# Performance work log

Hardware: AMD Instinct MI355X
Metric: run time of the kernel (lower is better)

The kernel has to match this reference:

```python
import jax, jax.numpy as jnp
import numpy as np

EMBED = 50
SEQ = 100
NLABEL = 15
HID = 20
VOCAB = 50000
BATCH = 8192


def gru_scan(xs, W, U, b, return_sequences):
    """Keras GRUCell (reset_after=True, gate order z,r,h).
    xs: (B, T, D). W: (D, 3H), U: (H, 3H), b: (2, 3H) [input bias, recurrent bias].
    """
    B = xs.shape[0]
    H = U.shape[0]
    bi, br = b[0], b[1]
    h0 = jnp.zeros((B, H), dtype=xs.dtype)

    def step(h, x_t):
        mx = x_t @ W + bi                      # (B, 3H)
        mh = h @ U + br                        # (B, 3H)
        xz, xr, xh = mx[:, :H], mx[:, H:2*H], mx[:, 2*H:]
        hz, hr, hh_ = mh[:, :H], mh[:, H:2*H], mh[:, 2*H:]
        z = jax.nn.sigmoid(xz + hz)
        r = jax.nn.sigmoid(xr + hr)
        hh = jnp.tanh(xh + r * hh_)
        h_new = z * h + (1.0 - z) * hh
        return h_new, h_new

    xs_t = jnp.swapaxes(xs, 0, 1)              # (T, B, D)
    h_last, hs = jax.lax.scan(step, h0, xs_t)
    if return_sequences:
        return jnp.swapaxes(hs, 0, 1)          # (B, T, H)
    return h_last                               # (B, H)


def setup_inputs() -> dict:
    key = jax.random.key(0)
    ks = jax.random.split(key, 9)
    s = 0.05
    return {
        "x": jax.random.randint(ks[0], (BATCH, SEQ), 0, VOCAB),
        "emb_table": jax.random.normal(ks[1], (VOCAB, EMBED), jnp.float32) * s,
        "W1": jax.random.normal(ks[2], (EMBED, 3 * HID), jnp.float32) * s,
        "U1": jax.random.normal(ks[3], (HID, 3 * HID), jnp.float32) * s,
        "b1": jnp.zeros((2, 3 * HID), jnp.float32),
        "W2": jax.random.normal(ks[4], (HID, 3 * HID), jnp.float32) * s,
        "U2": jax.random.normal(ks[5], (HID, 3 * HID), jnp.float32) * s,
        "b2": jnp.zeros((2, 3 * HID), jnp.float32),
        "Wd": jax.random.normal(ks[6], (HID, NLABEL), jnp.float32) * s,
        "bd": jnp.zeros((NLABEL,), jnp.float32),
        "drop_rate": 0,
    }


def reference(x, emb_table, W1, U1, b1, W2, U2, b2, Wd, bd, drop_rate):
    emb = emb_table[x]                               # (B, T, E)
    seq = gru_scan(emb, W1, U1, b1, return_sequences=True)   # (B, T, H)
    enc = gru_scan(seq, W2, U2, b2, return_sequences=False)  # (B, H)
    # drop_rate == 0 -> tf.nn.dropout is identity
    logits = enc @ Wd + bd                           # (B, 15)
    return logits
```

## Files before the change

kernel.cpp:

```cpp
#include <hip/hip_runtime.h>
#include <hip/hip_bf16.h>
#include <hip/hip_fp16.h>

#define SEQ_T 100
#define HID 20
#define EMB_D 50
#define VOCAB_N 50000
#define TABW 60
#define NTILE 3125
#define BBLK 782

typedef short sh8 __attribute__((ext_vector_type(8)));
typedef float f4  __attribute__((ext_vector_type(4)));

#define OFF_U1P 0
#define OFF_W2P 600
#define OFF_U2P 1200
#define OFF_B1  3600
#define OFF_B2  3720
#define OFF_WD  3840
#define OFF_BD  4140
#define OFF_TAB 4160

__device__ __forceinline__ float ldf(const void* p, int i, int isf) {
// ... 77 lines not shown
    bi[nt] = (col < TABW) ? ldf(b1, col, isf) : 0.f;
  }
  __syncthreads();

  for (int tile = wid; tile < NTILE; tile += BBLK * 4) {
    const int v0 = tile * 16;
    sh8 A0, A1;
#pragma unroll
    for (int jj = 0; jj < 8; ++jj) { A0[jj] = 0; A1[jj] = 0; }
    if (!isf) {
      const unsigned short* eb = (const unsigned short*)emb;
      const size_t rb = (size_t)(v0 + c) * EMB_D;
#pragma unroll
      for (int i = 0; i < 4; ++i) {
        unsigned d = *(const unsigned*)(eb + rb + q * 8 + 2 * i);
        A0[2 * i] = (short)(d & 0xffff); A0[2 * i + 1] = (short)(d >> 16);
      }
      const int k1b = 32 + q * 8;
#pragma unroll
      for (int i = 0; i < 4; ++i) {
        const int k = k1b + 2 * i;
        if (k + 1 < EMB_D) {
          unsigned d = *(const unsigned*)(eb + rb + k);
          A1[2 * i] = (short)(d & 0xffff); A1[2 * i + 1] = (short)(d >> 16);
        }
      }
    } else {
      const float* ef = (const float*)emb;
      const size_t rb = (size_t)(v0 + c) * EMB_D;
#pragma unroll
      for (int jj = 0; jj < 8; ++jj) {
        const int k0 = q * 8 + jj, k1 = 32 + q * 8 + jj;
        A0[jj] = f2bf(ef[rb + k0]);
        A1[jj] = (k1 < EMB_D) ? f2bf(ef[rb + k1]) : (short)0;
      }
    }
#pragma unroll
    for (int nt = 0; nt < 4; ++nt) {
      int4 b0i = sB[L][nt * 2], b1i = sB[L][nt * 2 + 1];
      sh8 B0 = *(const sh8*)&b0i, B1 = *(const sh8*)&b1i;
      const int col = nt * 16 + c;
      f4 acc = { bi[nt], bi[nt], bi[nt], bi[nt] };
      acc = __builtin_amdgcn_mfma_f32_16x16x32_bf16(A0, B0, acc, 0, 0, 0);
      acc = __builtin_amdgcn_mfma_f32_16x16x32_bf16(A1, B1, acc, 0, 0, 0);
      if (col < TABW) {
#pragma unroll
        for (int r = 0; r < 4; ++r)
          tab[(size_t)(v0 + q * 4 + r) * TABW + col] = acc[r];
      }
    }
  }
}

__global__ __launch_bounds__(256, 8) void gru_main(
    const int* __restrict__ x, const float* __restrict__ ws,
    const void* __restrict__ emb, void* __restrict__ out)
{
  const int isf = detect_isf(emb);
  const int j = threadIdx.x & 63;
  const int e = __builtin_amdgcn_readfirstlane(blockIdx.x * 4 + (threadIdx.x >> 6));
  const int jc = j < TABW ? j : 0;

  const int* xr = x + (size_t)e * SEQ_T;
  const float* tab = ws + OFF_TAB;
  const int o1 = jc * 40;
  const int jc4 = jc * 4;
  const int a1 = ((j - 20) & 63) * 4;
  const int a2 = ((j + 40) & 63) * 4;
  const float br1 = ws[OFF_B1 + 60 + jc];
  const float bi2 = ws[OFF_B2 + jc];
  const float br2 = ws[OFF_B2 + 60 + jc];
  float h2out;

  asm volatile(
    "global_load_dwordx4 v[10:13], %[o1], %[wsp] offset:0\n\t"
    "global_load_dwordx4 v[14:17], %[o1], %[wsp] offset:16\n\t"
    "global_load_dwordx2 v[18:19], %[o1], %[wsp] offset:32\n\t"
    "v_add_u32 v44, 0x960, %[o1]\n\t"
    "v_add_u32 v45, 0x12c0, %[o1]\n\t"
    "global_load_dwordx4 v[20:23], v44, %[wsp] offset:0\n\t"
    "global_load_dwordx4 v[24:27], v44, %[wsp] offset:16\n\t"
    "global_load_dwordx2 v[28:29], v44, %[wsp] offset:32\n\t"
    "global_load_dwordx4 v[30:33], v45, %[wsp] offset:0\n\t"
    "global_load_dwordx4 v[34:37], v45, %[wsp] offset:16\n\t"
    "global_load_dwordx2 v[38:39], v45, %[wsp] offset:32\n\t"
    "s_mov_b64 s[20:21], 0\n\ts_mov_b64 s[22:23], 0\n\t"
    "s_mov_b64 s[24:25], 0\n\ts_mov_b64 s[26:27], 0\n\t"
    "s_mov_b64 s[28:29], 0\n\t"
    "s_mov_b64 s[30:31], 0\n\ts_mov_b64 s[32:33], 0\n\t"
    "s_mov_b64 s[34:35], 0\n\ts_mov_b64 s[36:37], 0\n\t"
    "s_mov_b64 s[38:39], 0\n\t"
    "s_mov_b64 s[40:41], 0\n\ts_mov_b64 s[42:43], 0\n\t"
    "s_mov_b64 s[44:45], 0\n\ts_mov_b64 s[46:47], 0\n\t"
    "s_mov_b64 s[48:49], 0\n\t"
    "s_mov_b64 s[50:51], 0\n\ts_mov_b64 s[52:53], 0\n\t"
    "s_mov_b64 s[54:55], 0\n\ts_mov_b64 s[56:57], 0\n\t"
    "s_mov_b64 s[58:59], 0\n\t"
    "v_mov_b32 v40, 0\n\t"
    "v_mov_b32 v41, 0\n\t"
    "s_load_dword s65, %[xp], 0x0\n\t"
    "s_load_dword s66, %[xp], 0x4\n\t"
    "s_load_dword s68, %[xp], 0x8\n\t"
    "s_waitcnt lgkmcnt(0)\n\t"
    "s_mul_i32 s65, s65, 240\n\t"
    "s_mul_i32 s66, s66, 240\n\t"
    "s_mul_i32 s68, s68, 240\n\t"
    "v_add_u32 v50, s65, %[jc4]\n\t"
    "global_load_dword v53, v50, %[tabp]\n\t"
    "v_add_u32 v50, s66, %[jc4]\n\t"
    "global_load_dword v42, v50, %[tabp]\n\t"
    "v_add_u32 v50, s68, %[jc4]\n\t"
    "global_load_dword v43, v50, %[tabp]\n\t"
    "s_load_dword s65, %[xp], 0xc\n\t"
    "s_load_dword s68, %[xp], 0x10\n\t"
    "s_movk_i32 s64, 0x14\n\t"
    "s_movk_i32 s69, 0x18\n\t"
    "s_movk_i32 s67, 0x32\n\t"
    "s_waitcnt vmcnt(2)\n\t"
    "v_mov_b32 v44, %[br1]\n\t"
    "v_dot2_f32_f16 v44, s40, v10, v44\n\t"
    "v_dot2_f32_f16 v44, s41, v11, v44\n\t"
    "v_dot2_f32_f16 v44, s42, v12, v44\n\t"
    "v_dot2_f32_f16 v44, s43, v13, v44\n\t"
    "v_dot2_f32_f16 v44, s44, v14, v44\n\t"
    "v_dot2_f32_f16 v44, s45, v15, v44\n\t"
    "v_dot2_f32_f16 v44, s46, v16, v44\n\t"
    "v_dot2_f32_f16 v44, s47, v17, v44\n\t"
    "v_dot2_f32_f16 v44, s48, v18, v44\n\t"
    "v_dot2_f32_f16 v44, s49, v19, v44\n\t"
    "v_add_f32 v45, v53, v44\n\t"
    "v_mul_f32 v45, 0xbfb8aa3b, v45\n\t"
    "v_exp_f32 v45, v45\n\t"
    "s_nop 1\n\t"
    "v_add_f32 v45, 1.0, v45\n\t"
    "v_rcp_f32 v45, v45\n\t"
    "s_nop 1\n\t"
    "ds_bpermute_b32 v46, %[a1], v45\n\t"
    "s_waitcnt lgkmcnt(0)\n\t"
    "v_fma_f32 v47, v46, v44, v53\n\t"
    "v_mul_f32 v47, 0x4038aa3b, v47\n\t"
    "v_exp_f32 v47, v47\n\t"
    "s_nop 1\n\t"
    "v_add_f32 v47, 1.0, v47\n\t"
    "v_rcp_f32 v47, v47\n\t"
    "s_nop 1\n\t"
    "v_fma_f32 v47, -2.0, v47, 1.0\n\t"
    "ds_bpermute_b32 v46, %[a2], v47\n\t"
    "s_waitcnt lgkmcnt(0)\n\t"
    "v_sub_f32 v48, v40, v46\n\t"
    "v_fma_f32 v40, v45, v48, v46\n\t"
    "s_nop 1\n\t"
    "v_cvt_f16_f32 v46, v40\n\t"
    "s_nop 1\n\t"
    "ds_swizzle_b32 v47, v46 offset:0x041F\n\t"
    "s_waitcnt lgkmcnt(0)\n\t"
    "v_pack_b32_f16 v46, v46, v47\n\t"
    "s_nop 1\n\t"
    "v_readlane_b32 s20, v46, 0\n\t"
    "v_readlane_b32 s21, v46, 2\n\t"
    "v_readlane_b32 s22, v46, 4\n\t"
    "v_readlane_b32 s23, v46, 6\n\t"
    "v_readlane_b32 s24, v46, 8\n\t"
    "v_readlane_b32 s25, v46, 10\n\t"
    "v_readlane_b32 s26, v46, 12\n\t"
    "v_readlane_b32 s27, v46, 14\n\t"
    "v_readlane_b32 s28, v46, 16\n\t"
    "v_readlane_b32 s29, v46, 18\n\t"
    "0:\n\t"
    "v_mov_b32 v44, %[br1]\n\t"
    "v_mov_b32 v51, %[bi2]\n\t"
    "v_mov_b32 v52, %[br2]\n\t"
    "v_dot2_f32_f16 v44, s20, v10, v44\n\t"
    "v_dot2_f32_f16 v51, s20, v20, v51\n\t"
    "v_dot2_f32_f16 v52, s50, v30, v52\n\t"
    "v_dot2_f32_f16 v44, s21, v11, v44\n\t"
    "v_dot2_f32_f16 v51, s21, v21, v51\n\t"
    "v_dot2_f32_f16 v52, s51, v31, v52\n\t"
    "v_dot2_f32_f16 v44, s22, v12, v44\n\t"
    "v_dot2_f32_f16 v51, s22, v22, v51\n\t"
    "v_dot2_f32_f16 v52, s52, v32, v52\n\t"
    "v_dot2_f32_f16 v44, s23, v13, v44\n\t"
    "v_dot2_f32_f16 v51, s23, v23, v51\n\t"
    "v_dot2_f32_f16 v52, s53, v33, v52\n\t"
    "v_dot2_f32_f16 v44, s24, v14, v44\n\t"
    "v_dot2_f32_f16 v51, s24, v24, v51\n\t"
    "v_dot2_f32_f16 v52, s54, v34, v52\n\t"
    "v_dot2_f32_f16 v44, s25, v15, v44\n\t"
    "v_dot2_f32_f16 v51, s25, v25, v51\n\t"
    "v_dot2_f32_f16 v52, s55, v35, v52\n\t"
    "v_dot2_f32_f16 v44, s26, v16, v44\n\t"
    "v_dot2_f32_f16 v51, s26, v26, v51\n\t"
    "v_dot2_f32_f16 v52, s56, v36, v52\n\t"
    "v_dot2_f32_f16 v44, s27, v17, v44\n\t"
    "v_dot2_f32_f16 v51, s27, v27, v51\n\t"
    "v_dot2_f32_f16 v52, s57, v37, v52\n\t"
    "v_dot2_f32_f16 v44, s28, v18, v44\n\t"
    "v_dot2_f32_f16 v51, s28, v28, v51\n\t"
    "v_dot2_f32_f16 v52, s58, v38, v52\n\t"
    "v_dot2_f32_f16 v44, s29, v19, v44\n\t"
    "v_dot2_f32_f16 v51, s29, v29, v51\n\t"
    "v_dot2_f32_f16 v52, s59, v39, v52\n\t"
    "s_waitcnt vmcnt(1)\n\t"
    "v_add_f32 v45, v42, v44\n\t"
    "v_add_f32 v53, v51, v52\n\t"
    "v_mul_f32 v45, 0xbfb8aa3b, v45\n\t"
    "v_mul_f32 v53, 0xbfb8aa3b, v53\n\t"
    "v_exp_f32 v45, v45\n\t"
    "v_exp_f32 v53, v53\n\t"
    "v_add_f32 v45, 1.0, v45\n\t"
    "v_add_f32 v53, 1.0, v53\n\t"
    "v_rcp_f32 v45, v45\n\t"
    "v_rcp_f32 v53, v53\n\t"
    "ds_bpermute_b32 v46, %[a1], v45\n\t"
    "ds_bpermute_b32 v54, %[a1], v53\n\t"
    "s_mul_i32 s66, s65, 240\n\t"
    "v_add_u32 v50, s66, %[jc4]\n\t"
    "s_waitcnt lgkmcnt(0)\n\t"
    "v_fma_f32 v47, v46, v44, v42\n\t"
    "v_fma_f32 v55, v54, v52, v51\n\t"
    "global_load_dword v42, v50, %[tabp]\n\t"
    "v_mul_f32 v47, 0x4038aa3b, v47\n\t"
    "v_mul_f32 v55, 0x4038aa3b, v55\n\t"
    "v_exp_f32 v47, v47\n\t"
    "v_exp_f32 v55, v55\n\t"
    "v_add_f32 v47, 1.0, v47\n\t"
    "v_add_f32 v55, 1.0, v55\n\t"
    "v_rcp_f32 v47, v47\n\t"
    "v_rcp_f32 v55, v55\n\t"
    "v_fma_f32 v47, -2.0, v47, 1.0\n\t"
    "v_fma_f32 v55, -2.0, v55, 1.0\n\t"
    "ds_bpermute_b32 v46, %[a2], v47\n\t"
    "ds_bpermute_b32 v54, %[a2], v55\n\t"
    "s_waitcnt lgkmcnt(0)\n\t"
    "v_sub_f32 v48, v40, v46\n\t"
    "v_sub_f32 v51, v41, v54\n\t"
    "v_fma_f32 v40, v45, v48, v46\n\t"
    "v_fma_f32 v41, v53, v51, v54\n\t"
    "v_cvt_f16_f32 v46, v40\n\t"
    "v_cvt_f16_f32 v54, v41\n\t"
    "ds_swizzle_b32 v47, v46 offset:0x041F\n\t"
    "ds_swizzle_b32 v55, v54 offset:0x041F\n\t"
    "s_waitcnt lgkmcnt(0)\n\t"
    "v_pack_b32_f16 v46, v46, v47\n\t"
    "v_pack_b32_f16 v54, v54, v55\n\t"
    "s_min_u32 s64, s64, 396\n\t"
    "s_load_dword s65, %[xp], s64\n\t"
    "s_add_u32 s64, s64, 8\n\t"
    "s_nop 0\n\t"
    "v_readlane_b32 s40, v46, 0\n\t"
    "v_readlane_b32 s41, v46, 2\n\t"
    "v_readlane_b32 s42, v46, 4\n\t"
    "v_readlane_b32 s43, v46, 6\n\t"
    "v_readlane_b32 s44, v46, 8\n\t"
    "v_readlane_b32 s45, v46, 10\n\t"
    "v_readlane_b32 s46, v46, 12\n\t"
    "v_readlane_b32 s47, v46, 14\n\t"
    "v_readlane_b32 s48, v46, 16\n\t"
    "v_readlane_b32 s49, v46, 18\n\t"
    "v_readlane_b32 s30, v54, 0\n\t"
    "v_readlane_b32 s31, v54, 2\n\t"
    "v_readlane_b32 s32, v54, 4\n\t"
    "v_readlane_b32 s33, v54, 6\n\t"
    "v_readlane_b32 s34, v54, 8\n\t"
    "v_readlane_b32 s35, v54, 10\n\t"
    "v_readlane_b32 s36, v54, 12\n\t"
    "v_readlane_b32 s37, v54, 14\n\t"
    "v_readlane_b32 s38, v54, 16\n\t"
    "v_readlane_b32 s39, v54, 18\n\t"
    "v_mov_b32 v44, %[br1]\n\t"
    "v_mov_b32 v51, %[bi2]\n\t"
    "v_mov_b32 v52, %[br2]\n\t"
    "v_dot2_f32_f16 v44, s40, v10, v44\n\t"
    "v_dot2_f32_f16 v51, s40, v20, v51\n\t"
    "v_dot2_f32_f16 v52, s30, v30, v52\n\t"
    "v_dot2_f32_f16 v44, s41, v11, v44\n\t"
    "v_dot2_f32_f16 v51, s41, v21, v51\n\t"
    "v_dot2_f32_f16 v52, s31, v31, v52\n\t"
    "v_dot2_f32_f16 v44, s42, v12, v44\n\t"
    "v_dot2_f32_f16 v51, s42, v22, v51\n\t"
    "v_dot2_f32_f16 v52, s32, v32, v52\n\t"
    "v_dot2_f32_f16 v44, s43, v13, v44\n\t"
    "v_dot2_f32_f16 v51, s43, v23, v51\n\t"
    "v_dot2_f32_f16 v52, s33, v33, v52\n\t"
    "v_dot2_f32_f16 v44, s44, v14, v44\n\t"
    "v_dot2_f32_f16 v51, s44, v24, v51\n\t"
    "v_dot2_f32_f16 v52, s34, v34, v52\n\t"
    "v_dot2_f32_f16 v44, s45, v15, v44\n\t"
    "v_dot2_f32_f16 v51, s45, v25, v51\n\t"
    "v_dot2_f32_f16 v52, s35, v35, v52\n\t"
    "v_dot2_f32_f16 v44, s46, v16, v44\n\t"
    "v_dot2_f32_f16 v51, s46, v26, v51\n\t"
    "v_dot2_f32_f16 v52, s36, v36, v52\n\t"
    "v_dot2_f32_f16 v44, s47, v17, v44\n\t"
    "v_dot2_f32_f16 v51, s47, v27, v51\n\t"
    "v_dot2_f32_f16 v52, s37, v37, v52\n\t"
    "v_dot2_f32_f16 v44, s48, v18, v44\n\t"
    "v_dot2_f32_f16 v51, s48, v28, v51\n\t"
    "v_dot2_f32_f16 v52, s38, v38, v52\n\t"
    "v_dot2_f32_f16 v44, s49, v19, v44\n\t"
    "v_dot2_f32_f16 v51, s49, v29, v51\n\t"
    "v_dot2_f32_f16 v52, s39, v39, v52\n\t"
    "s_waitcnt vmcnt(1)\n\t"
    "v_add_f32 v45, v43, v44\n\t"
    "v_add_f32 v53, v51, v52\n\t"
    "v_mul_f32 v45, 0xbfb8aa3b, v45\n\t"
    "v_mul_f32 v53, 0xbfb8aa3b, v53\n\t"
    "v_exp_f32 v45, v45\n\t"
    "v_exp_f32 v53, v53\n\t"
    "v_add_f32 v45, 1.0, v45\n\t"
    "v_add_f32 v53, 1.0, v53\n\t"
    "v_rcp_f32 v45, v45\n\t"
    "v_rcp_f32 v53, v53\n\t"
    "ds_bpermute_b32 v46, %[a1], v45\n\t"
    "ds_bpermute_b32 v54, %[a1], v53\n\t"
    "s_mul_i32 s66, s68, 240\n\t"
    "v_add_u32 v50, s66, %[jc4]\n\t"
    "s_waitcnt lgkmcnt(0)\n\t"
    "v_fma_f32 v47, v46, v44, v43\n\t"
    "v_fma_f32 v55, v54, v52, v51\n\t"
    "global_load_dword v43, v50, %[tabp]\n\t"
    "v_mul_f32 v47, 0x4038aa3b, v47\n\t"
    "v_mul_f32 v55, 0x4038aa3b, v55\n\t"
    "v_exp_f32 v47, v47\n\t"
    "v_exp_f32 v55, v55\n\t"
    "v_add_f32 v47, 1.0, v47\n\t"
    "v_add_f32 v55, 1.0, v55\n\t"
    "v_rcp_f32 v47, v47\n\t"
    "v_rcp_f32 v55, v55\n\t"
    "v_fma_f32 v47, -2.0, v47, 1.0\n\t"
    "v_fma_f32 v55, -2.0, v55, 1.0\n\t"
    "ds_bpermute_b32 v46, %[a2], v47\n\t"
    "ds_bpermute_b32 v54, %[a2], v55\n\t"
    "s_waitcnt lgkmcnt(0)\n\t"
    "v_sub_f32 v48, v40, v46\n\t"
    "v_sub_f32 v51, v41, v54\n\t"
    "v_fma_f32 v40, v45, v48, v46\n\t"
    "v_fma_f32 v41, v53, v51, v54\n\t"
    "v_cvt_f16_f32 v46, v40\n\t"
    "v_cvt_f16_f32 v54, v41\n\t"
    "ds_swizzle_b32 v47, v46 offset:0x041F\n\t"
    "ds_swizzle_b32 v55, v54 offset:0x041F\n\t"
    "s_waitcnt lgkmcnt(0)\n\t"
    "v_pack_b32_f16 v46, v46, v47\n\t"
    "v_pack_b32_f16 v54, v54, v55\n\t"
    "s_min_u32 s69, s69, 392\n\t"
    "s_load_dword s68, %[xp], s69\n\t"
    "s_add_u32 s69, s69, 8\n\t"
    "s_nop 0\n\t"
    "v_readlane_b32 s20, v46, 0\n\t"
    "v_readlane_b32 s21, v46, 2\n\t"
    "v_readlane_b32 s22, v46, 4\n\t"
    "v_readlane_b32 s23, v46, 6\n\t"
    "v_readlane_b32 s24, v46, 8\n\t"
    "v_readlane_b32 s25, v46, 10\n\t"
    "v_readlane_b32 s26, v46, 12\n\t"
    "v_readlane_b32 s27, v46, 14\n\t"
    "v_readlane_b32 s28, v46, 16\n\t"
    "v_readlane_b32 s29, v46, 18\n\t"
    "v_readlane_b32 s50, v54, 0\n\t"
    "v_readlane_b32 s51, v54, 2\n\t"
    "v_readlane_b32 s52, v54, 4\n\t"
    "v_readlane_b32 s53, v54, 6\n\t"
    "v_readlane_b32 s54, v54, 8\n\t"
    "v_readlane_b32 s55, v54, 10\n\t"
    "v_readlane_b32 s56, v54, 12\n\t"
    "v_readlane_b32 s57, v54, 14\n\t"
    "v_readlane_b32 s58, v54, 16\n\t"
    "v_readlane_b32 s59, v54, 18\n\t"
    "s_sub_u32 s67, s67, 1\n\t"
    "s_cmp_lg_u32 s67, 0\n\t"
    "s_cbranch_scc1 0b\n\t"
    "s_waitcnt vmcnt(0) lgkmcnt(0)\n\t"
    "v_mov_b32 %[h2o], v41\n\t"
    : [h2o] "=v"(h2out)
    : [wsp] "s"(ws), [xp] "s"(xr), [tabp] "s"(tab),
      [o1] "v"(o1), [jc4] "v"(jc4), [a1] "v"(a1), [a2] "v"(a2),
      [br1] "v"(br1), [bi2] "v"(bi2), [br2] "v"(br2)
    : "memory", "vcc", "scc",
      "v10","v11","v12","v13","v14","v15","v16","v17","v18","v19",
      "v20","v21","v22","v23","v24","v25","v26","v27","v28","v29",
      "v30","v31","v32","v33","v34","v35","v36","v37","v38","v39",
      "v40","v41","v42","v43","v44","v45","v46","v47","v48","v49","v50",
      "v51","v52","v53","v54","v55",
      "s20","s21","s22","s23","s24","s25","s26","s27","s28","s29",
      "s30","s31","s32","s33","s34","s35","s36","s37","s38","s39",
      "s40","s41","s42","s43","s44","s45","s46","s47","s48","s49",
      "s50","s51","s52","s53","s54","s55","s56","s57","s58","s59",
      "s64","s65","s66","s67","s68","s69");

  if (j < 15) {
    float a = ws[OFF_BD + j];
#pragma unroll
    for (int k = 0; k < HID; ++k)
      a = fmaf(rdl(h2out, k), ws[OFF_WD + k * 15 + j], a);
    if (isf) ((float*)out)[(size_t)e * 15 + j] = a;
    else ((__hip_bfloat16*)out)[(size_t)e * 15 + j] = __float2bfloat16(a);
  }
}

extern "C" void kernel_launch(void* const* d_in, const int* in_sizes, int n_in,
                              void* d_out, int out_size, void* d_ws, size_t ws_size,
                              hipStream_t stream) {
  const int* x    = (const int*)d_in[0];
  const void* emb = d_in[1];
  const void* W1  = d_in[2];
  const void* U1  = d_in[3];
  const void* b1  = d_in[4];
  const void* W2  = d_in[5];
  const void* U2  = d_in[6];
  const void* b2  = d_in[7];
  const void* Wd  = d_in[8];
  const void* bd  = d_in[9];
  float* ws = (float*)d_ws;

  build_table<<<BBLK, 256, 0, stream>>>(
      emb, W1, b1, U1, W2, U2, b2, Wd, bd, ws);
  gru_main<<<2048, 256, 0, stream>>>(x, ws, emb, d_out);
}
```

Baseline: 232.7 us.

## Remap gate lanes so the z-gate crosses half-waves via permlane32 swap, not LDS bpermute

Reorders which wavefront lanes hold the z, r and candidate gate columns so the candidate sits in the upper half of the wave, aligned with the z-gate lanes. The second ds_bpermute is replaced with a masked v_permlane32_swap plus max, and the f16 neighbour swizzle is replaced with a DPP quad_perm move. The scalar readlanes then read lanes 32-50. The aim is to take LDS round-trips and lgkmcnt waits off the serial per-timestep critical path. The lane remapping is intricate and relies on the -4.0 sentinel and max trick being correct for every lane.

```diff
diff --git a/kernel.cpp b/kernel.cpp
--- a/kernel.cpp
+++ b/kernel.cpp
@@ -160,14 +160,20 @@
   const int isf = detect_isf(emb);
   const int j = threadIdx.x & 63;
   const int e = __builtin_amdgcn_readfirstlane(blockIdx.x * 4 + (threadIdx.x >> 6));
-  const int jc = j < TABW ? j : 0;
+
+  int jc;
+  if (j < 32)      jc = j;
+  else if (j < 52) jc = j + 8;
+  else if (j < 60) jc = j - 20;
+  else             jc = 0;
 
   const int* xr = x + (size_t)e * SEQ_T;
   const float* tab = ws + OFF_TAB;
   const int o1 = jc * 40;
   const int jc4 = jc * 4;
-  const int a1 = ((j - 20) & 63) * 4;
-  const int a2 = ((j + 40) & 63) * 4;
+  int src = 0;
+  if (j >= 32 && j < 52) { int cc = j - 32; src = (cc < 12) ? 20 + cc : 40 + cc; }
+  const int a1 = src * 4;
   const float br1 = ws[OFF_B1 + 60 + jc];
   const float bi2 = ws[OFF_B2 + jc];
   const float br2 = ws[OFF_B2 + 60 + jc];
@@ -185,6 +191,8 @@
     "global_load_dwordx4 v[30:33], v45, %[wsp] offset:0\n\t"
     "global_load_dwordx4 v[34:37], v45, %[wsp] offset:16\n\t"
     "global_load_dwordx2 v[38:39], v45, %[wsp] offset:32\n\t"
+    "s_mov_b32 s60, 0xfffff\n\t"
+    "s_mov_b32 s61, 0\n\t"
     "s_mov_b64 s[20:21], 0\n\ts_mov_b64 s[22:23], 0\n\t"
     "s_mov_b64 s[24:25], 0\n\ts_mov_b64 s[26:27], 0\n\t"
     "s_mov_b64 s[28:29], 0\n\t"
@@ -246,27 +254,30 @@
     "v_rcp_f32 v47, v47\n\t"
     "s_nop 1\n\t"
     "v_fma_f32 v47, -2.0, v47, 1.0\n\t"
-    "ds_bpermute_b32 v46, %[a2], v47\n\t"
-    "s_waitcnt lgkmcnt(0)\n\t"
-    "v_sub_f32 v48, v40, v46\n\t"
-    "v_fma_f32 v40, v45, v48, v46\n\t"
-    "s_nop 1\n\t"
+    "v_cndmask_b32 v46, -4.0, v45, s[60:61]\n\t"
+    "v_mov_b32 v48, v46\n\t"
+    "s_nop 1\n\t"
+    "v_permlane32_swap_b32 v46, v48\n\t"
+    "s_nop 1\n\t"
+    "v_max_f32 v46, v46, v48\n\t"
+    "v_sub_f32 v48, v40, v47\n\t"
+    "v_fma_f32 v40, v46, v48, v47\n\t"
     "v_cvt_f16_f32 v46, v40\n\t"
     "s_nop 1\n\t"
-    "ds_swizzle_b32 v47, v46 offset:0x041F\n\t"
-    "s_waitcnt lgkmcnt(0)\n\t"
-    "v_pack_b32_f16 v46, v46, v47\n\t"
-    "s_nop 1\n\t"
-    "v_readlane_b32 s20, v46, 0\n\t"
-    "v_readlane_b32 s21, v46, 2\n\t"
-    "v_readlane_b32 s22, v46, 4\n\t"
-    "v_readlane_b32 s23, v46, 6\n\t"
-    "v_readlane_b32 s24, v46, 8\n\t"
-    "v_readlane_b32 s25, v46, 10\n\t"
-    "v_readlane_b32 s26, v46, 12\n\t"
-    "v_readlane_b32 s27, v46, 14\n\t"
-    "v_readlane_b32 s28, v46, 16\n\t"
-    "v_readlane_b32 s29, v46, 18\n\t"
+    "v_mov_b32_dpp v48, v46 quad_perm:[1,0,3,2] row_mask:0xf bank_mask:0xf\n\t"
+    "s_nop 1\n\t"
+    "v_pack_b32_f16 v46, v46, v48\n\t"
+    "s_nop 1\n\t"
+    "v_readlane_b32 s20, v46, 32\n\t"
+    "v_readlane_b32 s21, v46, 34\n\t"
+    "v_readlane_b32 s22, v46, 36\n\t"
+    "v_readlane_b32 s23, v46, 38\n\t"
+    "v_readlane_b32 s24, v46, 40\n\t"
+    "v_readlane_b32 s25, v46, 42\n\t"
+    "v_readlane_b32 s26, v46, 44\n\t"
+    "v_readlane_b32 s27, v46, 46\n\t"
+    "v_readlane_b32 s28, v46, 48\n\t"
+    "v_readlane_b32 s29, v46, 50\n\t"
     "0:\n\t"
     "v_mov_b32 v44, %[br1]\n\t"
     "v_mov_b32 v51, %[bi2]\n\t"
@@ -320,6 +331,9 @@
     "v_fma_f32 v47, v46, v44, v42\n\t"
     "v_fma_f32 v55, v54, v52, v51\n\t"
     "global_load_dword v42, v50, %[tabp]\n\t"
+    "s_min_u32 s64, s64, 396\n\t"
+    "s_load_dword s65, %[xp], s64\n\t"
+    "s_add_u32 s64, s64, 8\n\t"
     "v_mul_f32 v47, 0x4038aa3b, v47\n\t"
     "v_mul_f32 v55, 0x4038aa3b, v55\n\t"
     "v_exp_f32 v47, v47\n\t"
@@ -328,46 +342,52 @@
     "v_add_f32 v55, 1.0, v55\n\t"
     "v_rcp_f32 v47, v47\n\t"
     "v_rcp_f32 v55, v55\n\t"
+    "s_nop 0\n\t"
     "v_fma_f32 v47, -2.0, v47, 1.0\n\t"
     "v_fma_f32 v55, -2.0, v55, 1.0\n\t"
-    "ds_bpermute_b32 v46, %[a2], v47\n\t"
-    "ds_bpermute_b32 v54, %[a2], v55\n\t"
-    "s_waitcnt lgkmcnt(0)\n\t"
-    "v_sub_f32 v48, v40, v46\n\t"
-    "v_sub_f32 v51, v41, v54\n\t"
-    "v_fma_f32 v40, v45, v48, v46\n\t"
-    "v_fma_f32 v41, v53, v51, v54\n\t"
+    "v_cndmask_b32 v46, -4.0, v45, s[60:61]\n\t"
+    "v_cndmask_b32 v54, -4.0, v53, s[60:61]\n\t"
+    "v_mov_b32 v48, v46\n\t"
+    "v_mov_b32 v59, v54\n\t"
+    "s_nop 1\n\t"
+    "v_permlane32_swap_b32 v46, v48\n\t"
+    "v_permlane32_swap_b32 v54, v59\n\t"
+    "s_nop 1\n\t"
+    "v_max_f32 v46, v46, v48\n\t"
+    "v_max_f32 v54, v54, v59\n\t"
+    "v_sub_f32 v48, v40, v47\n\t"
+    "v_fma_f32 v40, v46, v48, v47\n\t"
+    "v_sub_f32 v48, v41, v55\n\t"
+    "v_fma_f32 v41, v54, v48, v55\n\t"
     "v_cvt_f16_f32 v46, v40\n\t"
-    "v_cvt_f16_f32 v54, v41\n\t"
-    "ds_swizzle_b32 v47, v46 offset:0x041F\n\t"
-    "ds_swizzle_b32 v55, v54 offset:0x041F\n\t"
-    "s_waitcnt lgkmcnt(0)\n\t"
-    "v_pack_b32_f16 v46, v46, v47\n\t"
-    "v_pack_b32_f16 v54, v54, v55\n\t"
-    "s_min_u32 s64, s64, 396\n\t"
-    "s_load_dword s65, %[xp], s64\n\t"
-    "s_add_u32 s64, s64, 8\n\t"
-    "s_nop 0\n\t"
-    "v_readlane_b32 s40, v46, 0\n\t"
-    "v_readlane_b32 s41, v46, 2\n\t"
-    "v_readlane_b32 s42, v46, 4\n\t"
-    "v_readlane_b32 s43, v46, 6\n\t"
-    "v_readlane_b32 s44, v46, 8\n\t"
-    "v_readlane_b32 s45, v46, 10\n\t"
-    "v_readlane_b32 s46, v46, 12\n\t"
-    "v_readlane_b32 s47, v46, 14\n\t"
-    "v_readlane_b32 s48, v46, 16\n\t"
-    "v_readlane_b32 s49, v46, 18\n\t"
-    "v_readlane_b32 s30, v54, 0\n\t"
-    "v_readlane_b32 s31, v54, 2\n\t"
-    "v_readlane_b32 s32, v54, 4\n\t"
-    "v_readlane_b32 s33, v54, 6\n\t"
-    "v_readlane_b32 s34, v54, 8\n\t"
-    "v_readlane_b32 s35, v54, 10\n\t"
-    "v_readlane_b32 s36, v54, 12\n\t"
-    "v_readlane_b32 s37, v54, 14\n\t"
-    "v_readlane_b32 s38, v54, 16\n\t"
-    "v_readlane_b32 s39, v54, 18\n\t"
+    "v_cvt_f16_f32 v47, v41\n\t"
+    "s_nop 1\n\t"
+    "v_mov_b32_dpp v48, v46 quad_perm:[1,0,3,2] row_mask:0xf bank_mask:0xf\n\t"
+    "v_mov_b32_dpp v49, v47 quad_perm:[1,0,3,2] row_mask:0xf bank_mask:0xf\n\t"
+    "s_nop 1\n\t"
+    "v_pack_b32_f16 v46, v46, v48\n\t"
+    "v_pack_b32_f16 v47, v47, v49\n\t"
+    "s_nop 1\n\t"
+    "v_readlane_b32 s40, v46, 32\n\t"
+    "v_readlane_b32 s41, v46, 34\n\t"
+    "v_readlane_b32 s42, v46, 36\n\t"
+    "v_readlane_b32 s43, v46, 38\n\t"
+    "v_readlane_b32 s44, v46, 40\n\t"
+    "v_readlane_b32 s45, v46, 42\n\t"
+    "v_readlane_b32 s46, v46, 44\n\t"
+    "v_readlane_b32 s47, v46, 46\n\t"
+    "v_readlane_b32 s48, v46, 48\n\t"
+    "v_readlane_b32 s49, v46, 50\n\t"
+    "v_readlane_b32 s30, v47, 32\n\t"
+    "v_readlane_b32 s31, v47, 34\n\t"
+    "v_readlane_b32 s32, v47, 36\n\t"
+    "v_readlane_b32 s33, v47, 38\n\t"
+    "v_readlane_b32 s34, v47, 40\n\t"
+    "v_readlane_b32 s35, v47, 42\n\t"
+    "v_readlane_b32 s36, v47, 44\n\t"
+    "v_readlane_b32 s37, v47, 46\n\t"
+    "v_readlane_b32 s38, v47, 48\n\t"
+    "v_readlane_b32 s39, v47, 50\n\t"
     "v_mov_b32 v44, %[br1]\n\t"
     "v_mov_b32 v51, %[bi2]\n\t"
     "v_mov_b32 v52, %[br2]\n\t"
@@ -420,6 +440,9 @@
     "v_fma_f32 v47, v46, v44, v43\n\t"
     "v_fma_f32 v55, v54, v52, v51\n\t"
     "global_load_dword v43, v50, %[tabp]\n\t"
+    "s_min_u32 s69, s69, 392\n\t"
+    "s_load_dword s68, %[xp], s69\n\t"
+    "s_add_u32 s69, s69, 8\n\t"
     "v_mul_f32 v47, 0x4038aa3b, v47\n\t"
     "v_mul_f32 v55, 0x4038aa3b, v55\n\t"
     "v_exp_f32 v47, v47\n\t"
@@ -428,46 +451,52 @@
     "v_add_f32 v55, 1.0, v55\n\t"
     "v_rcp_f32 v47, v47\n\t"
     "v_rcp_f32 v55, v55\n\t"
+    "s_nop 0\n\t"
     "v_fma_f32 v47, -2.0, v47, 1.0\n\t"
     "v_fma_f32 v55, -2.0, v55, 1.0\n\t"
-    "ds_bpermute_b32 v46, %[a2], v47\n\t"
-    "ds_bpermute_b32 v54, %[a2], v55\n\t"
-    "s_waitcnt lgkmcnt(0)\n\t"
-    "v_sub_f32 v48, v40, v46\n\t"
-    "v_sub_f32 v51, v41, v54\n\t"
-    "v_fma_f32 v40, v45, v48, v46\n\t"
-    "v_fma_f32 v41, v53, v51, v54\n\t"
+    "v_cndmask_b32 v46, -4.0, v45, s[60:61]\n\t"
+    "v_cndmask_b32 v54, -4.0, v53, s[60:61]\n\t"
+    "v_mov_b32 v48, v46\n\t"
+    "v_mov_b32 v59, v54\n\t"
+    "s_nop 1\n\t"
+    "v_permlane32_swap_b32 v46, v48\n\t"
+    "v_permlane32_swap_b32 v54, v59\n\t"
+    "s_nop 1\n\t"
+    "v_max_f32 v46, v46, v48\n\t"
+    "v_max_f32 v54, v54, v59\n\t"
+    "v_sub_f32 v48, v40, v47\n\t"
+    "v_fma_f32 v40, v46, v48, v47\n\t"
+    "v_sub_f32 v48, v41, v55\n\t"
+    "v_fma_f32 v41, v54, v48, v55\n\t"
     "v_cvt_f16_f32 v46, v40\n\t"
-    "v_cvt_f16_f32 v54, v41\n\t"
-    "ds_swizzle_b32 v47, v46 offset:0x041F\n\t"
-    "ds_swizzle_b32 v55, v54 offset:0x041F\n\t"
-    "s_waitcnt lgkmcnt(0)\n\t"
-    "v_pack_b32_f16 v46, v46, v47\n\t"
-    "v_pack_b32_f16 v54, v54, v55\n\t"
-    "s_min_u32 s69, s69, 392\n\t"
-    "s_load_dword s68, %[xp], s69\n\t"
-    "s_add_u32 s69, s69, 8\n\t"
-    "s_nop 0\n\t"
-    "v_readlane_b32 s20, v46, 0\n\t"
-    "v_readlane_b32 s21, v46, 2\n\t"
-    "v_readlane_b32 s22, v46, 4\n\t"
-    "v_readlane_b32 s23, v46, 6\n\t"
-    "v_readlane_b32 s24, v46, 8\n\t"
-    "v_readlane_b32 s25, v46, 10\n\t"
-    "v_readlane_b32 s26, v46, 12\n\t"
-    "v_readlane_b32 s27, v46, 14\n\t"
-    "v_readlane_b32 s28, v46, 16\n\t"
-    "v_readlane_b32 s29, v46, 18\n\t"
-    "v_readlane_b32 s50, v54, 0\n\t"
-    "v_readlane_b32 s51, v54, 2\n\t"
-    "v_readlane_b32 s52, v54, 4\n\t"
-    "v_readlane_b32 s53, v54, 6\n\t"
-    "v_readlane_b32 s54, v54, 8\n\t"
-    "v_readlane_b32 s55, v54, 10\n\t"
-    "v_readlane_b32 s56, v54, 12\n\t"
-    "v_readlane_b32 s57, v54, 14\n\t"
-    "v_readlane_b32 s58, v54, 16\n\t"
-    "v_readlane_b32 s59, v54, 18\n\t"
+    "v_cvt_f16_f32 v47, v41\n\t"
+    "s_nop 1\n\t"
+    "v_mov_b32_dpp v48, v46 quad_perm:[1,0,3,2] row_mask:0xf bank_mask:0xf\n\t"
+    "v_mov_b32_dpp v49, v47 quad_perm:[1,0,3,2] row_mask:0xf bank_mask:0xf\n\t"
+    "s_nop 1\n\t"
+    "v_pack_b32_f16 v46, v46, v48\n\t"
+    "v_pack_b32_f16 v47, v47, v49\n\t"
+    "s_nop 1\n\t"
+    "v_readlane_b32 s20, v46, 32\n\t"
+    "v_readlane_b32 s21, v46, 34\n\t"
+    "v_readlane_b32 s22, v46, 36\n\t"
+    "v_readlane_b32 s23, v46, 38\n\t"
+    "v_readlane_b32 s24, v46, 40\n\t"
+    "v_readlane_b32 s25, v46, 42\n\t"
+    "v_readlane_b32 s26, v46, 44\n\t"
+    "v_readlane_b32 s27, v46, 46\n\t"
+    "v_readlane_b32 s28, v46, 48\n\t"
+    "v_readlane_b32 s29, v46, 50\n\t"
+    "v_readlane_b32 s50, v47, 32\n\t"
+    "v_readlane_b32 s51, v47, 34\n\t"
+    "v_readlane_b32 s52, v47, 36\n\t"
+    "v_readlane_b32 s53, v47, 38\n\t"
+    "v_readlane_b32 s54, v47, 40\n\t"
+    "v_readlane_b32 s55, v47, 42\n\t"
+    "v_readlane_b32 s56, v47, 44\n\t"
+    "v_readlane_b32 s57, v47, 46\n\t"
+    "v_readlane_b32 s58, v47, 48\n\t"
+    "v_readlane_b32 s59, v47, 50\n\t"
     "s_sub_u32 s67, s67, 1\n\t"
     "s_cmp_lg_u32 s67, 0\n\t"
     "s_cbranch_scc1 0b\n\t"
@@ -475,25 +504,25 @@
     "v_mov_b32 %[h2o], v41\n\t"
     : [h2o] "=v"(h2out)
     : [wsp] "s"(ws), [xp] "s"(xr), [tabp] "s"(tab),
-      [o1] "v"(o1), [jc4] "v"(jc4), [a1] "v"(a1), [a2] "v"(a2),
+      [o1] "v"(o1), [jc4] "v"(jc4), [a1] "v"(a1),
       [br1] "v"(br1), [bi2] "v"(bi2), [br2] "v"(br2)
     : "memory", "vcc", "scc",
       "v10","v11","v12","v13","v14","v15","v16","v17","v18","v19",
       "v20","v21","v22","v23","v24","v25","v26","v27","v28","v29",
       "v30","v31","v32","v33","v34","v35","v36","v37","v38","v39",
       "v40","v41","v42","v43","v44","v45","v46","v47","v48","v49","v50",
-      "v51","v52","v53","v54","v55",
+      "v51","v52","v53","v54","v55","v59",
       "s20","s21","s22","s23","s24","s25","s26","s27","s28","s29",
       "s30","s31","s32","s33","s34","s35","s36","s37","s38","s39",
       "s40","s41","s42","s43","s44","s45","s46","s47","s48","s49",
       "s50","s51","s52","s53","s54","s55","s56","s57","s58","s59",
-      "s64","s65","s66","s67","s68","s69");
+      "s60","s61","s64","s65","s66","s67","s68","s69");
 
   if (j < 15) {
     float a = ws[OFF_BD + j];
 #pragma unroll
     for (int k = 0; k < HID; ++k)
-      a = fmaf(rdl(h2out, k), ws[OFF_WD + k * 15 + j], a);
+      a = fmaf(rdl(h2out, 32 + k), ws[OFF_WD + k * 15 + j], a);
     if (isf) ((float*)out)[(size_t)e * 15 + j] = a;
     else ((__hip_bfloat16*)out)[(size_t)e * 15 + j] = __float2bfloat16(a);
   }
```

After: 243.5 us. 1.05x slower.

## Broadcast hidden state via LDS write/read instead of swizzle and readlanes

Applied to the files above, without the earlier changes.

Replaces the per-step hidden-state broadcast, which used ds_swizzle, pack and twenty v_readlane into SGPRs, with each lane writing its fp16 h value to a per-wave LDS slot and all lanes reading it back as vector registers. The dot products now take VGPR operands instead of SGPRs, and the x-index scalar loads move earlier in the step. This removes the serial readlane chain and SGPR dependencies, at the cost of LDS round-trip latency and about twenty extra VGPRs. The occupancy hint in launch_bounds is also dropped.

```diff
diff --git a/kernel.cpp b/kernel.cpp
--- a/kernel.cpp
+++ b/kernel.cpp
@@ -153,7 +153,7 @@
   }
 }
 
-__global__ __launch_bounds__(256, 8) void gru_main(
+__global__ __launch_bounds__(256) void gru_main(
     const int* __restrict__ x, const float* __restrict__ ws,
     const void* __restrict__ emb, void* __restrict__ out)
 {
@@ -171,6 +171,11 @@
   const float br1 = ws[OFF_B1 + 60 + jc];
   const float bi2 = ws[OFF_B2 + jc];
   const float br2 = ws[OFF_B2 + 60 + jc];
+
+  __shared__ char sbuf[1024];
+  const unsigned lb = (unsigned)(uintptr_t)&sbuf[0] + (threadIdx.x >> 6) * 256;
+  const int wad = (int)(lb + (j < 20 ? 2 * j : 40 + 2 * (j - 20)));
+  const int rad = (int)lb;
   float h2out;
 
   asm volatile(
@@ -185,20 +190,13 @@
     "global_load_dwordx4 v[30:33], v45, %[wsp] offset:0\n\t"
     "global_load_dwordx4 v[34:37], v45, %[wsp] offset:16\n\t"
     "global_load_dwordx2 v[38:39], v45, %[wsp] offset:32\n\t"
-    "s_mov_b64 s[20:21], 0\n\ts_mov_b64 s[22:23], 0\n\t"
-    "s_mov_b64 s[24:25], 0\n\ts_mov_b64 s[26:27], 0\n\t"
-    "s_mov_b64 s[28:29], 0\n\t"
-    "s_mov_b64 s[30:31], 0\n\ts_mov_b64 s[32:33], 0\n\t"
-    "s_mov_b64 s[34:35], 0\n\ts_mov_b64 s[36:37], 0\n\t"
-    "s_mov_b64 s[38:39], 0\n\t"
-    "s_mov_b64 s[40:41], 0\n\ts_mov_b64 s[42:43], 0\n\t"
-    "s_mov_b64 s[44:45], 0\n\ts_mov_b64 s[46:47], 0\n\t"
-    "s_mov_b64 s[48:49], 0\n\t"
-    "s_mov_b64 s[50:51], 0\n\ts_mov_b64 s[52:53], 0\n\t"
-    "s_mov_b64 s[54:55], 0\n\ts_mov_b64 s[56:57], 0\n\t"
-    "s_mov_b64 s[58:59], 0\n\t"
     "v_mov_b32 v40, 0\n\t"
     "v_mov_b32 v41, 0\n\t"
+    "v_mov_b32 v70, 0\n\tv_mov_b32 v71, 0\n\t"
+    "v_mov_b32 v72, 0\n\tv_mov_b32 v73, 0\n\t"
+    "v_mov_b32 v74, 0\n\tv_mov_b32 v75, 0\n\t"
+    "v_mov_b32 v76, 0\n\tv_mov_b32 v77, 0\n\t"
+    "v_mov_b32 v78, 0\n\tv_mov_b32 v79, 0\n\t"
     "s_load_dword s65, %[xp], 0x0\n\t"
     "s_load_dword s66, %[xp], 0x4\n\t"
     "s_load_dword s68, %[xp], 0x8\n\t"
@@ -207,7 +205,7 @@
     "s_mul_i32 s66, s66, 240\n\t"
     "s_mul_i32 s68, s68, 240\n\t"
     "v_add_u32 v50, s65, %[jc4]\n\t"
-    "global_load_dword v53, v50, %[tabp]\n\t"
+    "global_load_dword v52, v50, %[tabp]\n\t"
     "v_add_u32 v50, s66, %[jc4]\n\t"
     "global_load_dword v42, v50, %[tabp]\n\t"
     "v_add_u32 v50, s68, %[jc4]\n\t"
@@ -219,17 +217,7 @@
     "s_movk_i32 s67, 0x32\n\t"
     "s_waitcnt vmcnt(2)\n\t"
     "v_mov_b32 v44, %[br1]\n\t"
-    "v_dot2_f32_f16 v44, s40, v10, v44\n\t"
-    "v_dot2_f32_f16 v44, s41, v11, v44\n\t"
-    "v_dot2_f32_f16 v44, s42, v12, v44\n\t"
-    "v_dot2_f32_f16 v44, s43, v13, v44\n\t"
-    "v_dot2_f32_f16 v44, s44, v14, v44\n\t"
-    "v_dot2_f32_f16 v44, s45, v15, v44\n\t"
-    "v_dot2_f32_f16 v44, s46, v16, v44\n\t"
-    "v_dot2_f32_f16 v44, s47, v17, v44\n\t"
-    "v_dot2_f32_f16 v44, s48, v18, v44\n\t"
-    "v_dot2_f32_f16 v44, s49, v19, v44\n\t"
-    "v_add_f32 v45, v53, v44\n\t"
+    "v_add_f32 v45, v52, v44\n\t"
     "v_mul_f32 v45, 0xbfb8aa3b, v45\n\t"
     "v_exp_f32 v45, v45\n\t"
     "s_nop 1\n\t"
@@ -238,7 +226,7 @@
     "s_nop 1\n\t"
     "ds_bpermute_b32 v46, %[a1], v45\n\t"
     "s_waitcnt lgkmcnt(0)\n\t"
-    "v_fma_f32 v47, v46, v44, v53\n\t"
+    "v_fma_f32 v47, v46, v44, v52\n\t"
     "v_mul_f32 v47, 0x4038aa3b, v47\n\t"
     "v_exp_f32 v47, v47\n\t"
     "s_nop 1\n\t"
@@ -250,57 +238,46 @@
     "s_waitcnt lgkmcnt(0)\n\t"
     "v_sub_f32 v48, v40, v46\n\t"
     "v_fma_f32 v40, v45, v48, v46\n\t"
-    "s_nop 1\n\t"
     "v_cvt_f16_f32 v46, v40\n\t"
-    "s_nop 1\n\t"
-    "ds_swizzle_b32 v47, v46 offset:0x041F\n\t"
-    "s_waitcnt lgkmcnt(0)\n\t"
-    "v_pack_b32_f16 v46, v46, v47\n\t"
-    "s_nop 1\n\t"
-    "v_readlane_b32 s20, v46, 0\n\t"
-    "v_readlane_b32 s21, v46, 2\n\t"
-    "v_readlane_b32 s22, v46, 4\n\t"
-    "v_readlane_b32 s23, v46, 6\n\t"
-    "v_readlane_b32 s24, v46, 8\n\t"
-    "v_readlane_b32 s25, v46, 10\n\t"
-    "v_readlane_b32 s26, v46, 12\n\t"
-    "v_readlane_b32 s27, v46, 14\n\t"
-    "v_readlane_b32 s28, v46, 16\n\t"
-    "v_readlane_b32 s29, v46, 18\n\t"
+    "ds_write_b16 %[wad], v46\n\t"
+    "ds_read_b128 v[60:63], %[rad]\n\t"
+    "ds_read_b128 v[64:67], %[rad] offset:16\n\t"
+    "ds_read_b64  v[68:69], %[rad] offset:32\n\t"
     "0:\n\t"
     "v_mov_b32 v44, %[br1]\n\t"
     "v_mov_b32 v51, %[bi2]\n\t"
     "v_mov_b32 v52, %[br2]\n\t"
-    "v_dot2_f32_f16 v44, s20, v10, v44\n\t"
-    "v_dot2_f32_f16 v51, s20, v20, v51\n\t"
-    "v_dot2_f32_f16 v52, s50, v30, v52\n\t"
-    "v_dot2_f32_f16 v44, s21, v11, v44\n\t"
-    "v_dot2_f32_f16 v51, s21, v21, v51\n\t"
-    "v_dot2_f32_f16 v52, s51, v31, v52\n\t"
-    "v_dot2_f32_f16 v44, s22, v12, v44\n\t"
-    "v_dot2_f32_f16 v51, s22, v22, v51\n\t"
-    "v_dot2_f32_f16 v52, s52, v32, v52\n\t"
-    "v_dot2_f32_f16 v44, s23, v13, v44\n\t"
-    "v_dot2_f32_f16 v51, s23, v23, v51\n\t"
-    "v_dot2_f32_f16 v52, s53, v33, v52\n\t"
-    "v_dot2_f32_f16 v44, s24, v14, v44\n\t"
-    "v_dot2_f32_f16 v51, s24, v24, v51\n\t"
-    "v_dot2_f32_f16 v52, s54, v34, v52\n\t"
-    "v_dot2_f32_f16 v44, s25, v15, v44\n\t"
-    "v_dot2_f32_f16 v51, s25, v25, v51\n\t"
-    "v_dot2_f32_f16 v52, s55, v35, v52\n\t"
-    "v_dot2_f32_f16 v44, s26, v16, v44\n\t"
-    "v_dot2_f32_f16 v51, s26, v26, v51\n\t"
-    "v_dot2_f32_f16 v52, s56, v36, v52\n\t"
-    "v_dot2_f32_f16 v44, s27, v17, v44\n\t"
-    "v_dot2_f32_f16 v51, s27, v27, v51\n\t"
-    "v_dot2_f32_f16 v52, s57, v37, v52\n\t"
-    "v_dot2_f32_f16 v44, s28, v18, v44\n\t"
-    "v_dot2_f32_f16 v51, s28, v28, v51\n\t"
-    "v_dot2_f32_f16 v52, s58, v38, v52\n\t"
-    "v_dot2_f32_f16 v44, s29, v19, v44\n\t"
-    "v_dot2_f32_f16 v51, s29, v29, v51\n\t"
-    "v_dot2_f32_f16 v52, s59, v39, v52\n\t"
+    "s_waitcnt lgkmcnt(0)\n\t"
+    "v_dot2_f32_f16 v44, v60, v10, v44\n\t"
+    "v_dot2_f32_f16 v51, v60, v20, v51\n\t"
+    "v_dot2_f32_f16 v52, v70, v30, v52\n\t"
+    "v_dot2_f32_f16 v44, v61, v11, v44\n\t"
+    "v_dot2_f32_f16 v51, v61, v21, v51\n\t"
+    "v_dot2_f32_f16 v52, v71, v31, v52\n\t"
+    "v_dot2_f32_f16 v44, v62, v12, v44\n\t"
+    "v_dot2_f32_f16 v51, v62, v22, v51\n\t"
+    "v_dot2_f32_f16 v52, v72, v32, v52\n\t"
+    "v_dot2_f32_f16 v44, v63, v13, v44\n\t"
+    "v_dot2_f32_f16 v51, v63, v23, v51\n\t"
+    "v_dot2_f32_f16 v52, v73, v33, v52\n\t"
+    "v_dot2_f32_f16 v44, v64, v14, v44\n\t"
+    "v_dot2_f32_f16 v51, v64, v24, v51\n\t"
+    "v_dot2_f32_f16 v52, v74, v34, v52\n\t"
+    "v_dot2_f32_f16 v44, v65, v15, v44\n\t"
+    "v_dot2_f32_f16 v51, v65, v25, v51\n\t"
+    "v_dot2_f32_f16 v52, v75, v35, v52\n\t"
+    "v_dot2_f32_f16 v44, v66, v16, v44\n\t"
+    "v_dot2_f32_f16 v51, v66, v26, v51\n\t"
+    "v_dot2_f32_f16 v52, v76, v36, v52\n\t"
+    "v_dot2_f32_f16 v44, v67, v17, v44\n\t"
+    "v_dot2_f32_f16 v51, v67, v27, v51\n\t"
+    "v_dot2_f32_f16 v52, v77, v37, v52\n\t"
+    "v_dot2_f32_f16 v44, v68, v18, v44\n\t"
+    "v_dot2_f32_f16 v51, v68, v28, v51\n\t"
+    "v_dot2_f32_f16 v52, v78, v38, v52\n\t"
+    "v_dot2_f32_f16 v44, v69, v19, v44\n\t"
+    "v_dot2_f32_f16 v51, v69, v29, v51\n\t"
+    "v_dot2_f32_f16 v52, v79, v39, v52\n\t"
     "s_waitcnt vmcnt(1)\n\t"
     "v_add_f32 v45, v42, v44\n\t"
     "v_add_f32 v53, v51, v52\n\t"
@@ -320,6 +297,9 @@
     "v_fma_f32 v47, v46, v44, v42\n\t"
     "v_fma_f32 v55, v54, v52, v51\n\t"
     "global_load_dword v42, v50, %[tabp]\n\t"
+    "s_min_u32 s64, s64, 396\n\t"
+    "s_load_dword s65, %[xp], s64\n\t"
+    "s_add_u32 s64, s64, 8\n\t"
     "v_mul_f32 v47, 0x4038aa3b, v47\n\t"
     "v_mul_f32 v55, 0x4038aa3b, v55\n\t"
     "v_exp_f32 v47, v47\n\t"
@@ -328,79 +308,60 @@
     "v_add_f32 v55, 1.0, v55\n\t"
     "v_rcp_f32 v47, v47\n\t"
     "v_rcp_f32 v55, v55\n\t"
+    "s_nop 0\n\t"
     "v_fma_f32 v47, -2.0, v47, 1.0\n\t"
     "v_fma_f32 v55, -2.0, v55, 1.0\n\t"
     "ds_bpermute_b32 v46, %[a2], v47\n\t"
     "ds_bpermute_b32 v54, %[a2], v55\n\t"
     "s_waitcnt lgkmcnt(0)\n\t"
     "v_sub_f32 v48, v40, v46\n\t"
-    "v_sub_f32 v51, v41, v54\n\t"
     "v_fma_f32 v40, v45, v48, v46\n\t"
-    "v_fma_f32 v41, v53, v51, v54\n\t"
+    "v_sub_f32 v48, v41, v54\n\t"
+    "v_fma_f32 v41, v53, v48, v54\n\t"
     "v_cvt_f16_f32 v46, v40\n\t"
     "v_cvt_f16_f32 v54, v41\n\t"
-    "ds_swizzle_b32 v47, v46 offset:0x041F\n\t"
-    "ds_swizzle_b32 v55, v54 offset:0x041F\n\t"
-    "s_waitcnt lgkmcnt(0)\n\t"
-    "v_pack_b32_f16 v46, v46, v47\n\t"
-    "v_pack_b32_f16 v54, v54, v55\n\t"
-    "s_min_u32 s64, s64, 396\n\t"
-    "s_load_dword s65, %[xp], s64\n\t"
-    "s_add_u32 s64, s64, 8\n\t"
-    "s_nop 0\n\t"
-    "v_readlane_b32 s40, v46, 0\n\t"
-    "v_readlane_b32 s41, v46, 2\n\t"
-    "v_readlane_b32 s42, v46, 4\n\t"
-    "v_readlane_b32 s43, v46, 6\n\t"
-    "v_readlane_b32 s44, v46, 8\n\t"
-    "v_readlane_b32 s45, v46, 10\n\t"
-    "v_readlane_b32 s46, v46, 12\n\t"
-    "v_readlane_b32 s47, v46, 14\n\t"
-    "v_readlane_b32 s48, v46, 16\n\t"
-    "v_readlane_b32 s49, v46, 18\n\t"
-    "v_readlane_b32 s30, v54, 0\n\t"
-    "v_readlane_b32 s31, v54, 2\n\t"
-    "v_readlane_b32 s32, v54, 4\n\t"
-    "v_readlane_b32 s33, v54, 6\n\t"
-    "v_readlane_b32 s34, v54, 8\n\t"
-    "v_readlane_b32 s35, v54, 10\n\t"
-    "v_readlane_b32 s36, v54, 12\n\t"
-    "v_readlane_b32 s37, v54, 14\n\t"
-    "v_readlane_b32 s38, v54, 16\n\t"
-    "v_readlane_b32 s39, v54, 18\n\t"
+    "ds_write_b16 %[wad], v46\n\t"
+    "ds_write_b16 %[wad], v54 offset:128\n\t"
+    "ds_read_b128 v[60:63], %[rad]\n\t"
+    "ds_read_b128 v[64:67], %[rad] offset:16\n\t"
+    "ds_read_b64  v[68:69], %[rad] offset:32\n\t"
+    "ds_read_b128 v[70:73], %[rad] offset:128\n\t"
+    "ds_read_b128 v[74:77], %[rad] offset:144\n\t"
+    "ds_read_b64  v[78:79], %[rad] offset:160\n\t"
     "v_mov_b32 v44, %[br1]\n\t"
     "v_mov_b32 v51, %[bi2]\n\t"
     "v_mov_b32 v52, %[br2]\n\t"
-    "v_dot2_f32_f16 v44, s40, v10, v44\n\t"
-    "v_dot2_f32_f16 v51, s40, v20, v51\n\t"
-    "v_dot2_f32_f16 v52, s30, v30, v52\n\t"
-    "v_dot2_f32_f16 v44, s41, v11, v44\n\t"
-    "v_dot2_f32_f16 v51, s41, v21, v51\n\t"
-    "v_dot2_f32_f16 v52, s31, v31, v52\n\t"
-    "v_dot2_f32_f16 v44, s42, v12, v44\n\t"
-    "v_dot2_f32_f16 v51, s42, v22, v51\n\t"
-    "v_dot2_f32_f16 v52, s32, v32, v52\n\t"
-    "v_dot2_f32_f16 v44, s43, v13, v44\n\t"
-    "v_dot2_f32_f16 v51, s43, v23, v51\n\t"
-    "v_dot2_f32_f16 v52, s33, v33, v52\n\t"
-    "v_dot2_f32_f16 v44, s44, v14, v44\n\t"
-    "v_dot2_f32_f16 v51, s44, v24, v51\n\t"
-    "v_dot2_f32_f16 v52, s34, v34, v52\n\t"
-    "v_dot2_f32_f16 v44, s45, v15, v44\n\t"
-    "v_dot2_f32_f16 v51, s45, v25, v51\n\t"
-    "v_dot2_f32_f16 v52, s35, v35, v52\n\t"
-    "v_dot2_f32_f16 v44, s46, v16, v44\n\t"
-    "v_dot2_f32_f16 v51, s46, v26, v51\n\t"
-    "v_dot2_f32_f16 v52, s36, v36, v52\n\t"
-    "v_dot2_f32_f16 v44, s47, v17, v44\n\t"
-    "v_dot2_f32_f16 v51, s47, v27, v51\n\t"
-    "v_dot2_f32_f16 v52, s37, v37, v52\n\t"
-    "v_dot2_f32_f16 v44, s48, v18, v44\n\t"
-    "v_dot2_f32_f16 v51, s48, v28, v51\n\t"
-    "v_dot2_f32_f16 v52, s38, v38, v52\n\t"
-    "v_dot2_f32_f16 v44, s49, v19, v44\n\t"
-    "v_dot2_f32_f16 v51, s49, v29, v51\n\t"
-    "v_dot2_f32_f16 v52, s39, v39, v52\n\t"
+    "s_waitcnt lgkmcnt(0)\n\t"
+    "v_dot2_f32_f16 v44, v60, v10, v44\n\t"
+    "v_dot2_f32_f16 v51, v60, v20, v51\n\t"
+    "v_dot2_f32_f16 v52, v70, v30, v52\n\t"
+    "v_dot2_f32_f16 v44, v61, v11, v44\n\t"
+    "v_dot2_f32_f16 v51, v61, v21, v51\n\t"
+    "v_dot2_f32_f16 v52, v71, v31, v52\n\t"
+    "v_dot2_f32_f16 v44, v62, v12, v44\n\t"
+    "v_dot2_f32_f16 v51, v62, v22, v51\n\t"
+    "v_dot2_f32_f16 v52, v72, v32, v52\n\t"
+    "v_dot2_f32_f16 v44, v63, v13, v44\n\t"
+    "v_dot2_f32_f16 v51, v63, v23, v51\n\t"
+    "v_dot2_f32_f16 v52, v73, v33, v52\n\t"
+    "v_dot2_f32_f16 v44, v64, v14, v44\n\t"
+    "v_dot2_f32_f16 v51, v64, v24, v51\n\t"
+    "v_dot2_f32_f16 v52, v74, v34, v52\n\t"
+    "v_dot2_f32_f16 v44, v65, v15, v44\n\t"
+    "v_dot2_f32_f16 v51, v65, v25, v51\n\t"
+    "v_dot2_f32_f16 v52, v75, v35, v52\n\t"
+    "v_dot2_f32_f16 v44, v66, v16, v44\n\t"
+    "v_dot2_f32_f16 v51, v66, v26, v51\n\t"
+    "v_dot2_f32_f16 v52, v76, v36, v52\n\t"
+    "v_dot2_f32_f16 v44, v67, v17, v44\n\t"
+    "v_dot2_f32_f16 v51, v67, v27, v51\n\t"
+    "v_dot2_f32_f16 v52, v77, v37, v52\n\t"
+    "v_dot2_f32_f16 v44, v68, v18, v44\n\t"
+    "v_dot2_f32_f16 v51, v68, v28, v51\n\t"
+    "v_dot2_f32_f16 v52, v78, v38, v52\n\t"
+    "v_dot2_f32_f16 v44, v69, v19, v44\n\t"
+    "v_dot2_f32_f16 v51, v69, v29, v51\n\t"
+    "v_dot2_f32_f16 v52, v79, v39, v52\n\t"
     "s_waitcnt vmcnt(1)\n\t"
     "v_add_f32 v45, v43, v44\n\t"
     "v_add_f32 v53, v51, v52\n\t"
@@ -420,6 +381,9 @@
     "v_fma_f32 v47, v46, v44, v43\n\t"
     "v_fma_f32 v55, v54, v52, v51\n\t"
     "global_load_dword v43, v50, %[tabp]\n\t"
+    "s_min_u32 s69, s69, 392\n\t"
+    "s_load_dword s68, %[xp], s69\n\t"
+    "s_add_u32 s69, s69, 8\n\t"
     "v_mul_f32 v47, 0x4038aa3b, v47\n\t"
     "v_mul_f32 v55, 0x4038aa3b, v55\n\t"
     "v_exp_f32 v47, v47\n\t"
@@ -428,46 +392,26 @@
     "v_add_f32 v55, 1.0, v55\n\t"
     "v_rcp_f32 v47, v47\n\t"
     "v_rcp_f32 v55, v55\n\t"
+    "s_nop 0\n\t"
     "v_fma_f32 v47, -2.0, v47, 1.0\n\t"
     "v_fma_f32 v55, -2.0, v55, 1.0\n\t"
     "ds_bpermute_b32 v46, %[a2], v47\n\t"
     "ds_bpermute_b32 v54, %[a2], v55\n\t"
     "s_waitcnt lgkmcnt(0)\n\t"
     "v_sub_f32 v48, v40, v46\n\t"
-    "v_sub_f32 v51, v41, v54\n\t"
     "v_fma_f32 v40, v45, v48, v46\n\t"
-    "v_fma_f32 v41, v53, v51, v54\n\t"
+    "v_sub_f32 v48, v41, v54\n\t"
+    "v_fma_f32 v41, v53, v48, v54\n\t"
     "v_cvt_f16_f32 v46, v40\n\t"
     "v_cvt_f16_f32 v54, v41\n\t"
-    "ds_swizzle_b32 v47, v46 offset:0x041F\n\t"
-    "ds_swizzle_b32 v55, v54 offset:0x041F\n\t"
-    "s_waitcnt lgkmcnt(0)\n\t"
-    "v_pack_b32_f16 v46, v46, v47\n\t"
-    "v_pack_b32_f16 v54, v54, v55\n\t"
-    "s_min_u32 s69, s69, 392\n\t"
-    "s_load_dword s68, %[xp], s69\n\t"
-    "s_add_u32 s69, s69, 8\n\t"
-    "s_nop 0\n\t"
-    "v_readlane_b32 s20, v46, 0\n\t"
-    "v_readlane_b32 s21, v46, 2\n\t"
-    "v_readlane_b32 s22, v46, 4\n\t"
-    "v_readlane_b32 s23, v46, 6\n\t"
-    "v_readlane_b32 s24, v46, 8\n\t"
-    "v_readlane_b32 s25, v46, 10\n\t"
-    "v_readlane_b32 s26, v46, 12\n\t"
-    "v_readlane_b32 s27, v46, 14\n\t"
-    "v_readlane_b32 s28, v46, 16\n\t"
-    "v_readlane_b32 s29, v46, 18\n\t"
-    "v_readlane_b32 s50, v54, 0\n\t"
-    "v_readlane_b32 s51, v54, 2\n\t"
-    "v_readlane_b32 s52, v54, 4\n\t"
-    "v_readlane_b32 s53, v54, 6\n\t"
-    "v_readlane_b32 s54, v54, 8\n\t"
-    "v_readlane_b32 s55, v54, 10\n\t"
-    "v_readlane_b32 s56, v54, 12\n\t"
-    "v_readlane_b32 s57, v54, 14\n\t"
-    "v_readlane_b32 s58, v54, 16\n\t"
-    "v_readlane_b32 s59, v54, 18\n\t"
+    "ds_write_b16 %[wad], v46\n\t"
+    "ds_write_b16 %[wad], v54 offset:128\n\t"
+    "ds_read_b128 v[60:63], %[rad]\n\t"
+    "ds_read_b128 v[64:67], %[rad] offset:16\n\t"
+    "ds_read_b64  v[68:69], %[rad] offset:32\n\t"
+    "ds_read_b128 v[70:73], %[rad] offset:128\n\t"
+    "ds_read_b128 v[74:77], %[rad] offset:144\n\t"
+    "ds_read_b64  v[78:79], %[rad] offset:160\n\t"
     "s_sub_u32 s67, s67, 1\n\t"
     "s_cmp_lg_u32 s67, 0\n\t"
     "s_cbranch_scc1 0b\n\t"
@@ -476,17 +420,16 @@
     : [h2o] "=v"(h2out)
     : [wsp] "s"(ws), [xp] "s"(xr), [tabp] "s"(tab),
       [o1] "v"(o1), [jc4] "v"(jc4), [a1] "v"(a1), [a2] "v"(a2),
-      [br1] "v"(br1), [bi2] "v"(bi2), [br2] "v"(br2)
+      [br1] "v"(br1), [bi2] "v"(bi2), [br2] "v"(br2),
+      [wad] "v"(wad), [rad] "v"(rad)
     : "memory", "vcc", "scc",
       "v10","v11","v12","v13","v14","v15","v16","v17","v18","v19",
       "v20","v21","v22","v23","v24","v25","v26","v27","v28","v29",
       "v30","v31","v32","v33","v34","v35","v36","v37","v38","v39",
-      "v40","v41","v42","v43","v44","v45","v46","v47","v48","v49","v50",
+      "v40","v41","v42","v43","v44","v45","v46","v47","v48","v50",
       "v51","v52","v53","v54","v55",
-      "s20","s21","s22","s23","s24","s25","s26","s27","s28","s29",
-      "s30","s31","s32","s33","s34","s35","s36","s37","s38","s39",
-      "s40","s41","s42","s43","s44","s45","s46","s47","s48","s49",
-      "s50","s51","s52","s53","s54","s55","s56","s57","s58","s59",
+      "v60","v61","v62","v63","v64","v65","v66","v67","v68","v69",
+      "v70","v71","v72","v73","v74","v75","v76","v77","v78","v79",
       "s64","s65","s66","s67","s68","s69");
 
   if (j < 15) {
```

Result: faster. 202.8 us (-12.9%).
